# Kernel optimization log

Measured on AMD Instinct MI355X. Metric: run time of the kernel, lower is better.

The kernel has to match this reference:

```python
import jax, jax.numpy as jnp
import numpy as np

DIM = 2048
K_DIM = 2048
HQ = 16          # query heads
HKV = 4          # kv heads
HD = DIM // HQ   # head dim = 128
KV_DIM = HD * HKV
MAX_LEN = 4096
THETA = 10000.0
ROPE_FACTOR = 8.0
CAUSAL = True
SCALE = HD ** -0.5


def rope_cos_sin(n):
    # mirrors generate_sin_cos_pos_emb (rope_factor > 1 branch)
    idx = jnp.arange(0, HD, 2, dtype=jnp.float32) / HD
    seq_len_eff = max(n, MAX_LEN)  # static python ints
    base_adjustment = (ROPE_FACTOR * seq_len_eff / MAX_LEN - (ROPE_FACTOR - 1.0)) ** (HD / (HD - 2))
    inv_freq = 1.0 / (THETA * base_adjustment) ** idx
    pos = jnp.arange(n, dtype=jnp.float32)
    if not CAUSAL:
        pos = pos - (n - 1) // 2
    freqs = pos[:, None] * inv_freq[None, :]          # [n, HD/2]
    emb = jnp.concatenate([freqs, freqs], axis=-1)    # [n, HD]
    return jnp.cos(emb), jnp.sin(emb)


def rotate_half(x):
    x1, x2 = jnp.split(x, 2, axis=-1)
    return jnp.concatenate([-x2, x1], axis=-1)


def setup_inputs() -> dict:
    key = jax.random.key(0)
    ks = jax.random.split(key, 11)
    B, N = 2, 2048
    s = 0.02
    return {
        "query": jax.random.normal(ks[0], (B, N, DIM), jnp.float32),
        "key": jax.random.normal(ks[1], (B, N, K_DIM), jnp.float32),
        "value": jax.random.normal(ks[2], (B, N, K_DIM), jnp.float32),
        "Wq": jax.random.normal(ks[3], (DIM, DIM), jnp.float32) * s,
        "bq": jnp.zeros((DIM,), jnp.float32),
        "Wk": jax.random.normal(ks[4], (KV_DIM, K_DIM), jnp.float32) * s,
        "bk": jnp.zeros((KV_DIM,), jnp.float32),
        "Wv": jax.random.normal(ks[5], (KV_DIM, K_DIM), jnp.float32) * s,
        "bv": jnp.zeros((KV_DIM,), jnp.float32),
        "Wo": jax.random.normal(ks[6], (DIM, DIM), jnp.float32) * s,
        "bo": jnp.zeros((DIM,), jnp.float32),
    }


def reference(query, key, value, Wq, bq, Wk, bk, Wv, bv, Wo, bo):
    b, n, _ = query.shape
    q = query @ Wq.T + bq                       # [b, n, DIM]
    k = key @ Wk.T + bk                         # [b, n, KV_DIM]
    v = value @ Wv.T + bv                       # [b, n, KV_DIM]
    q = q.reshape(b, n, HQ, HD).transpose(0, 2, 1, 3)    # [b, HQ, n, d]
    k = k.reshape(b, n, HKV, HD).transpose(0, 2, 1, 3)   # [b, HKV, n, d]
    v = v.reshape(b, n, HKV, HD).transpose(0, 2, 1, 3)
    cos, sin = rope_cos_sin(n)                  # [n, HD] each, broadcast over b,h
    q = q * cos + rotate_half(q) * sin
    k = k * cos + rotate_half(k) * sin
    g = HQ // HKV
    qg = q.reshape(b, HKV, g, n, HD)            # group query heads per kv head
    scores = jnp.einsum('bhgnd,bhsd->bhgns', qg * SCALE, k)  # [b, HKV, g, n, s]
    if CAUSAL:
        causal = jnp.tril(jnp.ones((n, n), dtype=bool))
        scores = jnp.where(causal[None, None, None], scores, jnp.finfo(scores.dtype).min)
    attn = jax.nn.softmax(scores, axis=-1)
    out = jnp.einsum('bhgns,bhsd->bhgnd', attn, v)           # [b, HKV, g, n, d]
    out = out.reshape(b, HQ, n, HD).transpose(0, 2, 1, 3).reshape(b, n, DIM)
    return out @ Wo.T + bo
```

## Files before the change

kernel.cpp:

```cpp
#include <hip/hip_runtime.h>
#include <cstdint>


typedef __bf16 bf16_t;
typedef __attribute__((ext_vector_type(8))) __bf16 bf16x8;
typedef __attribute__((ext_vector_type(4))) float f32x4;

#define B_    2
#define N_    2048
#define DIM_  2048
#define HQ_   16
#define HKV_  4
#define HD_   128
#define KVD_  512
#define SCALE_ 0.08838834764831845f

static __device__ __forceinline__ void ld_g2l(void* lds, const void* g) {
  __builtin_amdgcn_global_load_lds((__attribute__((address_space(1))) void*)g,
                                   (__attribute__((address_space(3))) void*)lds,
                                   16, 0, 0);
}

static __device__ __forceinline__ f32x4 vmax4(f32x4 a, f32x4 b) {
  f32x4 r;
  r[0] = fmaxf(a[0], b[0]); r[1] = fmaxf(a[1], b[1]);
  r[2] = fmaxf(a[2], b[2]); r[3] = fmaxf(a[3], b[3]);
  return r;
}

__global__ void k_prep(float* __restrict__ cosT, float* __restrict__ sinT,
                       const float* __restrict__ s0, bf16_t* __restrict__ d0, int n0,
                       const float* __restrict__ s1, bf16_t* __restrict__ d1, int n1,
                       const float* __restrict__ s2, bf16_t* __restrict__ d2, int n2,
                       const float* __restrict__ s3, bf16_t* __restrict__ d3, int n3)
{
  if (blockIdx.x < 512) {
    int idx = blockIdx.x * 256 + threadIdx.x;
    int i = idx & 63;
    int n = idx >> 6;
    float inv = expf(-(float)i * (9.210340371976184f / 64.0f));
    float ang = (float)n * inv;
    cosT[idx] = cosf(ang);
    sinT[idx] = sinf(ang);
    return;
  }
  int i = ((blockIdx.x - 512) * 256 + threadIdx.x) * 4;
  const float* s; bf16_t* d; int off;
  if (i < n0)                     { s = s0; d = d0; off = i; }
  else if (i < n0 + n1)           { s = s1; d = d1; off = i - n0; }
  else if (i < n0 + n1 + n2)      { s = s2; d = d2; off = i - n0 - n1; }
  else if (i < n0 + n1 + n2 + n3) { s = s3; d = d3; off = i - n0 - n1 - n2; }
  else return;
  f32x4 v = *(const f32x4*)(s + off);
  union { bf16_t h[4]; uint2 u; } pk;
  pk.h[0] = (bf16_t)v[0]; pk.h[1] = (bf16_t)v[1];
  pk.h[2] = (bf16_t)v[2]; pk.h[3] = (bf16_t)v[3];
  *(uint2*)(d + off) = pk.u;
}

__global__ __launch_bounds__(256, 2) void k_gemm_qkv(
    const float* __restrict__ q, const bf16_t* __restrict__ Wqb,
    const float* __restrict__ bq, bf16_t* __restrict__ Qp,
    const float* __restrict__ k, const bf16_t* __restrict__ Wkb,
    const float* __restrict__ bk, bf16_t* __restrict__ Kp,
    const float* __restrict__ v, const bf16_t* __restrict__ Wvb,
    const float* __restrict__ bv, bf16_t* __restrict__ Vp)
{
  __shared__ bf16_t As[128 * 64];
  __shared__ bf16_t Bs[2][128 * 64];
  const int z = blockIdx.z;
  if (z != 0 && blockIdx.y >= 2) return;
  const float* A; const bf16_t* W; const float* bias; bf16_t* C; int Nn;
  if (z == 0)      { A = q; W = Wqb; bias = bq; C = Qp; Nn = 2048; }
  else if (z == 1) { A = k; W = Wkb; bias = bk; C = Kp; Nn = 512; }
  else             { A = v; W = Wvb; bias = bv; C = Vp; Nn = 512; }

  const int tid  = threadIdx.x;
  const int lane = tid & 63;
  const int wave = tid >> 6;
  const int l15  = lane & 15;
  const int lg   = lane >> 4;
  const int bm = blockIdx.x;
  const int bn0 = blockIdx.y * 2, bn1 = bn0 + 1;
  const int wr = (wave >> 1) * 64, wc = (wave & 1) * 64;
  const int K = 2048;

  f32x4 acc0[4][4] = {};
  f32x4 acc1[4][4] = {};

  uint8_t* AsB = (uint8_t*)As;
  uint8_t* Bs0 = (uint8_t*)Bs[0];
  uint8_t* Bs1 = (uint8_t*)Bs[1];
  const uint8_t* Wb0 = (const uint8_t*)W + (size_t)(bn0 * 128) * K * 2;
  const uint8_t* Wb1 = (const uint8_t*)W + (size_t)(bn1 * 128) * K * 2;

  f32x4 arLo[4], arHi[4];

  auto loadA = [&](int k0) {
#pragma unroll
    for (int i = 0; i < 4; ++i) {
      int c = i * 256 + tid;
      int row = c >> 3;
      int k8  = (c & 7) * 8;
      const float* ap = A + (size_t)(bm * 128 + row) * K + k0 + k8;
      arLo[i] = *(const f32x4*)ap;
      arHi[i] = *(const f32x4*)(ap + 4);
    }
  };
  auto writeA = [&]() {
#pragma unroll
    for (int i = 0; i < 4; ++i) {
      int c = i * 256 + tid;
      int row = c >> 3;
      int k8  = (c & 7) * 8;
      bf16x8 va;
      f32x4 lo = arLo[i], hi = arHi[i];
      va[0] = (bf16_t)lo[0]; va[1] = (bf16_t)lo[1];
      va[2] = (bf16_t)lo[2]; va[3] = (bf16_t)lo[3];
      va[4] = (bf16_t)hi[0]; va[5] = (bf16_t)hi[1];
      va[6] = (bf16_t)hi[2]; va[7] = (bf16_t)hi[3];
      int sw = (k8 * 2) ^ ((row & 7) << 4);
      *(bf16x8*)(AsB + row * 128 + sw) = va;
    }
  };

  loadA(0);

  for (int k0 = 0; k0 < K; k0 += 64) {
#pragma unroll
    for (int r = 0; r < 4; ++r) {
      int o = r * 4096 + wave * 1024 + lane * 16;
      int row = o >> 7;
      int colB = (o & 127) ^ ((row & 7) << 4);
      size_t goff = (size_t)row * (K * 2) + (size_t)k0 * 2 + colB;
      ld_g2l(Bs0 + r * 4096 + wave * 1024, Wb0 + goff);
      ld_g2l(Bs1 + r * 4096 + wave * 1024, Wb1 + goff);
    }
    writeA();
    const bool more = (k0 + 64 < K);
    __syncthreads();
    if (more) loadA(k0 + 64);
    __builtin_amdgcn_s_setprio(1);
#pragma unroll
    for (int kk = 0; kk < 2; ++kk) {
      const int koff = kk * 64 + (lg << 4);
      bf16x8 fa[4], fb[4];
#pragma unroll
      for (int fi = 0; fi < 4; ++fi) {
        int row = wr + fi * 16 + l15;
        fa[fi] = *(const bf16x8*)(AsB + row * 128 + (koff ^ ((row & 7) << 4)));
      }
#pragma unroll
      for (int fj = 0; fj < 4; ++fj) {
        int row = wc + fj * 16 + l15;
        fb[fj] = *(const bf16x8*)(Bs0 + row * 128 + (koff ^ ((row & 7) << 4)));
      }
#pragma unroll
      for (int fi = 0; fi < 4; ++fi)
#pragma unroll
        for (int fj = 0; fj < 4; ++fj)
          acc0[fi][fj] = __builtin_amdgcn_mfma_f32_16x16x32_bf16(
              fa[fi], fb[fj], acc0[fi][fj], 0, 0, 0);
#pragma unroll
      for (int fj = 0; fj < 4; ++fj) {
        int row = wc + fj * 16 + l15;
        fb[fj] = *(const bf16x8*)(Bs1 + row * 128 + (koff ^ ((row & 7) << 4)));
      }
#pragma unroll
      for (int fi = 0; fi < 4; ++fi)
#pragma unroll
        for (int fj = 0; fj < 4; ++fj)
          acc1[fi][fj] = __builtin_amdgcn_mfma_f32_16x16x32_bf16(
              fa[fi], fb[fj], acc1[fi][fj], 0, 0, 0);
    }
    __builtin_amdgcn_s_setprio(0);
    __syncthreads();
  }

  const int r0 = lg * 4;
#pragma unroll
  for (int fi = 0; fi < 4; ++fi) {
#pragma unroll
    for (int rr = 0; rr < 4; ++rr) {
      int grow = bm * 128 + wr + fi * 16 + r0 + rr;
      size_t rowoff = (size_t)grow * Nn;
#pragma unroll
      for (int fj = 0; fj < 4; ++fj) {
        int gc0 = bn0 * 128 + wc + fj * 16 + l15;
        int gc1 = bn1 * 128 + wc + fj * 16 + l15;
        C[rowoff + gc0] = (bf16_t)(acc0[fi][fj][rr] + bias[gc0]);
        C[rowoff + gc1] = (bf16_t)(acc1[fi][fj][rr] + bias[gc1]);
      }
    }
  }
}

__global__ __launch_bounds__(256, 4) void k_gemm_o(
    const bf16_t* __restrict__ Ain, const bf16_t* __restrict__ Wob,
    const float* __restrict__ bo, float* __restrict__ out)
{
  __shared__ bf16_t As[128 * 64];
  __shared__ bf16_t Bs[128 * 64];
  const int tid  = threadIdx.x;
  const int lane = tid & 63;
  const int wave = tid >> 6;
  const int l15  = lane & 15;
  const int lg   = lane >> 4;
  const int bm = blockIdx.x, bn = blockIdx.y;
  const int wr = (wave >> 1) * 64, wc = (wave & 1) * 64;
  const int K = 2048, N = 2048;

  f32x4 acc[4][4] = {};
  uint8_t* AsB = (uint8_t*)As;
  uint8_t* BsB = (uint8_t*)Bs;
  const uint8_t* Wbase = (const uint8_t*)Wob + (size_t)(bn * 128) * K * 2;
  const uint8_t* Abase = (const uint8_t*)Ain + (size_t)(bm * 128) * K * 2;

  for (int k0 = 0; k0 < K; k0 += 64) {
    for (int r = 0; r < 4; ++r) {
      int o = r * 4096 + wave * 1024 + lane * 16;
      int row = o >> 7;
      int colB = (o & 127) ^ ((row & 7) << 4);
      size_t goff = (size_t)row * (K * 2) + (size_t)k0 * 2 + colB;
      ld_g2l(BsB + r * 4096 + wave * 1024, Wbase + goff);
      ld_g2l(AsB + r * 4096 + wave * 1024, Abase + goff);
    }
    __syncthreads();
    for (int kk = 0; kk < 2; ++kk) {
      const int koff = kk * 64 + (lg << 4);
      bf16x8 fa[4], fb[4];
      for (int fi = 0; fi < 4; ++fi) {
        int row = wr + fi * 16 + l15;
        fa[fi] = *(const bf16x8*)(AsB + row * 128 + (koff ^ ((row & 7) << 4)));
      }
      for (int fj = 0; fj < 4; ++fj) {
        int row = wc + fj * 16 + l15;
        fb[fj] = *(const bf16x8*)(BsB + row * 128 + (koff ^ ((row & 7) << 4)));
      }
      for (int fi = 0; fi < 4; ++fi)
        for (int fj = 0; fj < 4; ++fj)
          acc[fi][fj] = __builtin_amdgcn_mfma_f32_16x16x32_bf16(
              fa[fi], fb[fj], acc[fi][fj], 0, 0, 0);
    }
    __syncthreads();
  }

  const int r0 = lg * 4;
  for (int fi = 0; fi < 4; ++fi) {
    for (int rr = 0; rr < 4; ++rr) {
      int grow = bm * 128 + wr + fi * 16 + r0 + rr;
      size_t rowoff = (size_t)grow * N;
      for (int fj = 0; fj < 4; ++fj) {
        int gcol = bn * 128 + wc + fj * 16 + l15;
        out[rowoff + gcol] = acc[fi][fj][rr] + bo[gcol];
      }
    }
  }
}

__global__ void k_ropek_transv(bf16_t* __restrict__ Kp,
                               const float* __restrict__ cosT,
                               const float* __restrict__ sinT,
                               const bf16_t* __restrict__ Vp,
                               bf16_t* __restrict__ Vt)
{
  __shared__ bf16_t tile[64][72];
  const int tid = threadIdx.x;
  if (blockIdx.x < 512) {
    int idx = blockIdx.x * 256 + tid;
    int j = idx & 7;
    int h = (idx >> 3) & 3;
    int row = idx >> 5;
    int n = row & (N_ - 1);
    int d0 = j * 8;
    const float* cp = cosT + (n << 6) + d0;
    const float* sp = sinT + (n << 6) + d0;
    f32x4 c0 = *(const f32x4*)cp,  c1 = *(const f32x4*)(cp + 4);
    f32x4 s0 = *(const f32x4*)sp,  s1 = *(const f32x4*)(sp + 4);
    bf16_t* xb = Kp + (size_t)row * 512 + (h << 7) + d0;
    bf16x8 x1 = *(const bf16x8*)xb;
    bf16x8 x2 = *(const bf16x8*)(xb + 64);
    bf16x8 o1, o2;
#pragma unroll
    for (int e = 0; e < 8; ++e) {
      float c = e < 4 ? c0[e] : c1[e - 4];
      float s = e < 4 ? s0[e] : s1[e - 4];
      float a = (float)x1[e], bvl = (float)x2[e];
      o1[e] = (bf16_t)(a * c - bvl * s);
      o2[e] = (bf16_t)(bvl * c + a * s);
    }
    *(bf16x8*)xb = o1;
    *(bf16x8*)(xb + 64) = o2;
    return;
  }
  const int bid = blockIdx.x - 512;
  const int r0 = (bid & 63) * 64;
  const int d0 = (bid >> 6) * 64;
  for (int r = 0; r < 2; ++r) {
    int n = r * 32 + (tid >> 3);
    int dc = (tid & 7) * 8;
    *(uint4*)&tile[n][dc] = *(const uint4*)(Vp + (size_t)(r0 + n) * KVD_ + d0 + dc);
  }
  __syncthreads();
  const int b = r0 >> 11;
  const int nseq = r0 & (N_ - 1);
  for (int r = 0; r < 2; ++r) {
    int dd = r * 32 + (tid >> 3);
    int nc = (tid & 7) * 8;
    int dglob = d0 + dd;
    int hkv = dglob >> 7, dloc = dglob & 127;
    union { bf16_t h[8]; uint4 v; } pk;
    for (int j = 0; j < 8; ++j) pk.h[j] = tile[nc + j][dd];
    size_t drow = (size_t)(b * HKV_ + hkv) * 128 + dloc;
    *(uint4*)(Vt + drow * N_ + nseq + nc) = pk.v;
  }
}

__global__ __launch_bounds__(256, 2) void k_attn(
    const bf16_t* __restrict__ Qp, const bf16_t* __restrict__ Kp,
    const bf16_t* __restrict__ Vt, bf16_t* __restrict__ AO,
    const float* __restrict__ cosT, const float* __restrict__ sinT)
{
  __shared__ bf16_t Ks[2][64 * 128];
  __shared__ bf16_t Vs[2][128 * 64];
  __shared__ bf16_t Ps[4][16 * 72];
  const int tid = threadIdx.x, lane = tid & 63, wave = tid >> 6;
  const int l15 = lane & 15, lg = lane >> 4;
  const int bx = (blockIdx.y < 16) ? (15 - (int)blockIdx.x) : (int)blockIdx.x;
  const int qtile = bx * 4 + wave;
  const int bh = blockIdx.y;
  const int b = bh >> 4, hq = bh & 15, hkv = hq >> 2;

  bf16x8 qf[2][4];
#pragma unroll
  for (int rf = 0; rf < 2; ++rf) {
    int n = qtile * 32 + rf * 16 + l15;
    size_t qrow = (size_t)b * N_ + n;
    const uint8_t* qb = (const uint8_t*)Qp + (qrow * DIM_ + (size_t)hq * HD_) * 2 + lg * 16;
#pragma unroll
    for (int ks = 0; ks < 4; ++ks)
      qf[rf][ks] = *(const bf16x8*)(qb + ks * 64);
    const float* cb = cosT + n * 64 + lg * 8;
    const float* sb = sinT + n * 64 + lg * 8;
    f32x4 c0a = *(const f32x4*)cb,        c0b = *(const f32x4*)(cb + 4);
    f32x4 c1a = *(const f32x4*)(cb + 32), c1b = *(const f32x4*)(cb + 36);
    f32x4 s0a = *(const f32x4*)sb,        s0b = *(const f32x4*)(sb + 4);
    f32x4 s1a = *(const f32x4*)(sb + 32), s1b = *(const f32x4*)(sb + 36);
#pragma unroll
    for (int e = 0; e < 8; ++e) {
      float c0 = e < 4 ? c0a[e] : c0b[e - 4], s0 = e < 4 ? s0a[e] : s0b[e - 4];
      float c1 = e < 4 ? c1a[e] : c1b[e - 4], s1 = e < 4 ? s1a[e] : s1b[e - 4];
      float a0 = (float)qf[rf][0][e], b0 = (float)qf[rf][2][e];
      float a1 = (float)qf[rf][1][e], b1 = (float)qf[rf][3][e];
      qf[rf][0][e] = (bf16_t)((a0 * c0 - b0 * s0) * SCALE_);
      qf[rf][2][e] = (bf16_t)((b0 * c0 + a0 * s0) * SCALE_);
      qf[rf][1][e] = (bf16_t)((a1 * c1 - b1 * s1) * SCALE_);
      qf[rf][3][e] = (bf16_t)((b1 * c1 + a1 * s1) * SCALE_);
    }
  }

  float m[2] = {-1e30f, -1e30f};
  float ln[2] = {0.f, 0.f};
  f32x4 o[2][8] = {};

  const uint8_t* KpB = (const uint8_t*)Kp + ((size_t)b * N_ * KVD_ + (size_t)hkv * HD_) * 2;
  const uint8_t* VtB = (const uint8_t*)Vt + (size_t)(b * HKV_ + hkv) * HD_ * (size_t)N_ * 2;
  uint8_t* PwB = (uint8_t*)Ps[wave];

  const int Tw   = qtile / 2 + 1;
  const int Tmax = 2 * bx + 2;

  auto stage = [&](int buf, int t) {
    uint8_t* KsB = (uint8_t*)Ks[buf];
    uint8_t* VsB = (uint8_t*)Vs[buf];
#pragma unroll
    for (int r = 0; r < 4; ++r) {
      int o16 = r * 4096 + wave * 1024 + lane * 16;
      int row = o16 >> 8;
      int colB = (o16 & 255) ^ ((row & 7) << 4);
      ld_g2l(KsB + r * 4096 + wave * 1024,
             KpB + (size_t)(t * 64 + row) * (KVD_ * 2) + colB);
    }
#pragma unroll
    for (int r = 0; r < 4; ++r) {
      int o16 = r * 4096 + wave * 1024 + lane * 16;
      int dd = o16 >> 7;
      int colB = (o16 & 127) ^ ((dd & 7) << 4);
      ld_g2l(VsB + r * 4096 + wave * 1024,
             VtB + (size_t)dd * (N_ * 2) + t * 128 + colB);
    }
  };

  stage(0, 0);
  __syncthreads();
  int cur = 0;

  for (int t = 0; t < Tmax; ++t) {
    if (t + 1 < Tmax) stage(cur ^ 1, t + 1);

    if (t < Tw) {
      const uint8_t* KsB = (const uint8_t*)Ks[cur];
      const uint8_t* VsB = (const uint8_t*)Vs[cur];

      f32x4 s4[2][4] = {};
      __builtin_amdgcn_s_setprio(1);
#pragma unroll
      for (int ks = 0; ks < 4; ++ks) {
        int koff = ks * 64 + lg * 16;
#pragma unroll
        for (int kb = 0; kb < 4; ++kb) {
          int row = kb * 16 + l15;
          bf16x8 kf = *(const bf16x8*)(KsB + row * 256 + (koff ^ ((row & 7) << 4)));
          s4[0][kb] = __builtin_amdgcn_mfma_f32_16x16x32_bf16(kf, qf[0][ks], s4[0][kb], 0, 0, 0);
          s4[1][kb] = __builtin_amdgcn_mfma_f32_16x16x32_bf16(kf, qf[1][ks], s4[1][kb], 0, 0, 0);
        }
      }
      __builtin_amdgcn_s_setprio(0);

      if (t == Tw - 1) {
#pragma unroll
        for (int rf = 0; rf < 2; ++rf) {
          int q = qtile * 32 + rf * 16 + l15;
#pragma unroll
          for (int kb = 0; kb < 4; ++kb) {
            int key = t * 64 + kb * 16 + lg * 4;
#pragma unroll
            for (int rr = 0; rr < 4; ++rr)
              if (key + rr > q) s4[rf][kb][rr] = -1e30f;
          }
        }
      }

      bf16x8 pf[2][2];
#pragma unroll
      for (int rf = 0; rf < 2; ++rf) {
        f32x4 mx = vmax4(vmax4(s4[rf][0], s4[rf][1]), vmax4(s4[rf][2], s4[rf][3]));
        float rm = fmaxf(fmaxf(mx[0], mx[1]), fmaxf(mx[2], mx[3]));
        rm = fmaxf(rm, __shfl_xor(rm, 16));
        rm = fmaxf(rm, __shfl_xor(rm, 32));

        const bool defer = __all(rm <= m[rf] + 8.0f);
        float mn = defer ? m[rf] : fmaxf(m[rf], rm);
        float sc = defer ? 1.0f : __expf(m[rf] - mn);

        f32x4 p[4];
        f32x4 psum = {0.f, 0.f, 0.f, 0.f};
#pragma unroll
        for (int kb = 0; kb < 4; ++kb) {
#pragma unroll
          for (int rr = 0; rr < 4; ++rr)
            p[kb][rr] = __expf(s4[rf][kb][rr] - mn);
          psum += p[kb];
        }
        float rs = (psum[0] + psum[1]) + (psum[2] + psum[3]);
        rs += __shfl_xor(rs, 16);
        rs += __shfl_xor(rs, 32);
        ln[rf] = ln[rf] * sc + rs;
        m[rf] = mn;

        if (!defer) {
#pragma unroll
          for (int db = 0; db < 8; ++db) o[rf][db] *= sc;
        }

#pragma unroll
        for (int kb = 0; kb < 4; ++kb) {
          union { bf16_t h[4]; uint2 u; } pk;
          pk.h[0] = (bf16_t)p[kb][0]; pk.h[1] = (bf16_t)p[kb][1];
          pk.h[2] = (bf16_t)p[kb][2]; pk.h[3] = (bf16_t)p[kb][3];
          *(uint2*)(PwB + l15 * 144 + kb * 32 + lg * 8) = pk.u;
        }
        pf[rf][0] = *(const bf16x8*)(PwB + l15 * 144 + lg * 16);
        pf[rf][1] = *(const bf16x8*)(PwB + l15 * 144 + 64 + lg * 16);
      }

      __builtin_amdgcn_s_setprio(1);
#pragma unroll
      for (int ks2 = 0; ks2 < 2; ++ks2) {
        int koff = ks2 * 64 + lg * 16;
#pragma unroll
        for (int db = 0; db < 8; ++db) {
          int dd = db * 16 + l15;
          bf16x8 vf = *(const bf16x8*)(VsB + dd * 128 + (koff ^ ((dd & 7) << 4)));
          o[0][db] = __builtin_amdgcn_mfma_f32_16x16x32_bf16(vf, pf[0][ks2], o[0][db], 0, 0, 0);
          o[1][db] = __builtin_amdgcn_mfma_f32_16x16x32_bf16(vf, pf[1][ks2], o[1][db], 0, 0, 0);
        }
      }
      __builtin_amdgcn_s_setprio(0);
    }

    __syncthreads();
    cur ^= 1;
  }

#pragma unroll
  for (int rf = 0; rf < 2; ++rf) {
    float iv = 1.f / ln[rf];
    size_t qrow = (size_t)b * N_ + qtile * 32 + rf * 16 + l15;
    uint8_t* ob = (uint8_t*)(AO + qrow * DIM_ + (size_t)hq * HD_);
#pragma unroll
    for (int db = 0; db < 8; ++db) {
      union { bf16_t h[4]; uint2 u; } pk;
      pk.h[0] = (bf16_t)(o[rf][db][0] * iv);
      pk.h[1] = (bf16_t)(o[rf][db][1] * iv);
      pk.h[2] = (bf16_t)(o[rf][db][2] * iv);
      pk.h[3] = (bf16_t)(o[rf][db][3] * iv);
      *(uint2*)(ob + (db * 16 + lg * 4) * 2) = pk.u;
    }
  }
}

extern "C" void kernel_launch(void* const* d_in, const int* in_sizes, int n_in,
                              void* d_out, int out_size, void* d_ws, size_t ws_size,
                              hipStream_t stream)
{
  if (ws_size < (46u << 20)) return;

  const float* query = (const float*)d_in[0];
  const float* key   = (const float*)d_in[1];
  const float* value = (const float*)d_in[2];
  const float* Wq = (const float*)d_in[3];
  const float* bq = (const float*)d_in[4];
  const float* Wk = (const float*)d_in[5];
  const float* bk = (const float*)d_in[6];
  const float* Wv = (const float*)d_in[7];
  const float* bv = (const float*)d_in[8];
  const float* Wo = (const float*)d_in[9];
  const float* bo = (const float*)d_in[10];
  float* out = (float*)d_out;

  uint8_t* ws = (uint8_t*)d_ws;
  float*  cosT = (float*)(ws);
  float*  sinT = (float*)(ws + (512u << 10));
  bf16_t* Qp   = (bf16_t*)(ws + (1u  << 20));
  bf16_t* Kp   = (bf16_t*)(ws + (17u << 20));
  bf16_t* Vp   = (bf16_t*)(ws + (21u << 20));
  bf16_t* Vt   = (bf16_t*)(ws + (25u << 20));
  bf16_t* Wqb  = (bf16_t*)(ws + (29u << 20));
  bf16_t* Wkb  = (bf16_t*)(ws + (37u << 20));
  bf16_t* Wvb  = (bf16_t*)(ws + (39u << 20));
  bf16_t* WobL = (bf16_t*)(ws + (17u << 20));
  bf16_t* WobE = (bf16_t*)(ws + (41u << 20));

  const bool bigws = ws_size >= (50ull << 20);

  if (bigws) {
    k_prep<<<512 + 10240, 256, 0, stream>>>(cosT, sinT,
                                            Wq, Wqb, 4194304,
                                            Wk, Wkb, 1048576,
                                            Wv, Wvb, 1048576,
                                            Wo, WobE, 4194304);
  } else {
    k_prep<<<512 + 6144, 256, 0, stream>>>(cosT, sinT,
                                           Wq, Wqb, 4194304,
                                           Wk, Wkb, 1048576,
                                           Wv, Wvb, 1048576,
                                           nullptr, nullptr, 0);
  }

  k_gemm_qkv<<<dim3(32, 8, 3), 256, 0, stream>>>(
      query, Wqb, bq, Qp, key, Wkb, bk, Kp, value, Wvb, bv, Vp);

  k_ropek_transv<<<1024, 256, 0, stream>>>(Kp, cosT, sinT, Vp, Vt);

  k_attn<<<dim3(16, 32), 256, 0, stream>>>(Qp, Kp, Vt, Qp, cosT, sinT);

  if (!bigws) {
    k_prep<<<4096, 256, 0, stream>>>(nullptr, nullptr,
                                     Wo, WobL, 4194304,
                                     nullptr, nullptr, 0,
                                     nullptr, nullptr, 0,
                                     nullptr, nullptr, 0);
  }

  k_gemm_o<<<dim3(32, 16), 256, 0, stream>>>(
      Qp, bigws ? WobE : WobL, bo, out);
}
```

Baseline: 199.3 us.

## Fuse K RoPE and V transpose into QKV GEMM epilogue

Removes the separate RoPE-on-K and V-transpose kernel by doing both in the QKV projection's epilogue through an LDS staging tile. K blocks apply rotary embedding using the partner half read from shared memory, and V blocks write the transposed layout directly. This saves a kernel launch and a round trip of K and V through global memory, but it adds barriers and strided LDS reads to the GEMM epilogue. The small-workspace Wo buffer is moved so it no longer overlaps Kp.

```diff
diff --git a/kernel.cpp b/kernel.cpp
--- a/kernel.cpp
+++ b/kernel.cpp
@@ -64,16 +64,16 @@
     const float* __restrict__ k, const bf16_t* __restrict__ Wkb,
     const float* __restrict__ bk, bf16_t* __restrict__ Kp,
     const float* __restrict__ v, const bf16_t* __restrict__ Wvb,
-    const float* __restrict__ bv, bf16_t* __restrict__ Vp)
+    const float* __restrict__ bv, bf16_t* __restrict__ Vt,
+    const float* __restrict__ cosT, const float* __restrict__ sinT)
 {
-  __shared__ bf16_t As[128 * 64];
-  __shared__ bf16_t Bs[2][128 * 64];
+  __shared__ bf16_t smem[24576];
   const int z = blockIdx.z;
   if (z != 0 && blockIdx.y >= 2) return;
-  const float* A; const bf16_t* W; const float* bias; bf16_t* C; int Nn;
-  if (z == 0)      { A = q; W = Wqb; bias = bq; C = Qp; Nn = 2048; }
-  else if (z == 1) { A = k; W = Wkb; bias = bk; C = Kp; Nn = 512; }
-  else             { A = v; W = Wvb; bias = bv; C = Vp; Nn = 512; }
+  const float* A; const bf16_t* W; const float* bias;
+  if (z == 0)      { A = q; W = Wqb; bias = bq; }
+  else if (z == 1) { A = k; W = Wkb; bias = bk; }
+  else             { A = v; W = Wvb; bias = bv; }
 
   const int tid  = threadIdx.x;
   const int lane = tid & 63;
@@ -88,9 +88,9 @@
   f32x4 acc0[4][4] = {};
   f32x4 acc1[4][4] = {};
 
-  uint8_t* AsB = (uint8_t*)As;
-  uint8_t* Bs0 = (uint8_t*)Bs[0];
-  uint8_t* Bs1 = (uint8_t*)Bs[1];
+  uint8_t* AsB = (uint8_t*)smem;
+  uint8_t* Bs0 = AsB + 16384;
+  uint8_t* Bs1 = AsB + 32768;
   const uint8_t* Wb0 = (const uint8_t*)W + (size_t)(bn0 * 128) * K * 2;
   const uint8_t* Wb1 = (const uint8_t*)W + (size_t)(bn1 * 128) * K * 2;
 
@@ -178,20 +178,79 @@
   }
 
   const int r0 = lg * 4;
-#pragma unroll
-  for (int fi = 0; fi < 4; ++fi) {
-#pragma unroll
-    for (int rr = 0; rr < 4; ++rr) {
-      int grow = bm * 128 + wr + fi * 16 + r0 + rr;
-      size_t rowoff = (size_t)grow * Nn;
-#pragma unroll
-      for (int fj = 0; fj < 4; ++fj) {
-        int gc0 = bn0 * 128 + wc + fj * 16 + l15;
-        int gc1 = bn1 * 128 + wc + fj * 16 + l15;
-        C[rowoff + gc0] = (bf16_t)(acc0[fi][fj][rr] + bias[gc0]);
-        C[rowoff + gc1] = (bf16_t)(acc1[fi][fj][rr] + bias[gc1]);
-      }
-    }
+
+  if (z == 0) {
+#pragma unroll
+    for (int fi = 0; fi < 4; ++fi)
+#pragma unroll
+      for (int rr = 0; rr < 4; ++rr) {
+        int grow = bm * 128 + wr + fi * 16 + r0 + rr;
+        size_t rowoff = (size_t)grow * 2048;
+#pragma unroll
+        for (int fj = 0; fj < 4; ++fj) {
+          int gc0 = bn0 * 128 + wc + fj * 16 + l15;
+          int gc1 = bn1 * 128 + wc + fj * 16 + l15;
+          Qp[rowoff + gc0] = (bf16_t)(acc0[fi][fj][rr] + bias[gc0]);
+          Qp[rowoff + gc1] = (bf16_t)(acc1[fi][fj][rr] + bias[gc1]);
+        }
+      }
+    return;
+  }
+
+  bf16_t* T = smem;
+  const int nbase = (bm * 128) & (N_ - 1);
+  const int vb = (bm * 128) >> 11;
+
+  for (int t = 0; t < 2; ++t) {
+    const int bn = t == 0 ? bn0 : bn1;
+    f32x4 (&acc)[4][4] = t == 0 ? acc0 : acc1;
+
+#pragma unroll
+    for (int fi = 0; fi < 4; ++fi)
+#pragma unroll
+      for (int rr = 0; rr < 4; ++rr) {
+        int row = wr + fi * 16 + r0 + rr;
+#pragma unroll
+        for (int fj = 0; fj < 4; ++fj) {
+          int d = wc + fj * 16 + l15;
+          T[row * 132 + d] = (bf16_t)(acc[fi][fj][rr] + bias[bn * 128 + d]);
+        }
+      }
+    __syncthreads();
+
+    if (z == 1) {
+#pragma unroll
+      for (int fi = 0; fi < 4; ++fi)
+#pragma unroll
+        for (int rr = 0; rr < 4; ++rr) {
+          int row = wr + fi * 16 + r0 + rr;
+          int grow = bm * 128 + row;
+          int n = grow & (N_ - 1);
+#pragma unroll
+          for (int fj = 0; fj < 4; ++fj) {
+            int d = wc + fj * 16 + l15;
+            float own = acc[fi][fj][rr] + bias[bn * 128 + d];
+            float p = (float)T[row * 132 + (d ^ 64)];
+            int di = d & 63;
+            float c = cosT[n * 64 + di];
+            float s = sinT[n * 64 + di];
+            float outv = (d < 64) ? (own * c - p * s) : (own * c + p * s);
+            Kp[(size_t)grow * KVD_ + bn * 128 + d] = (bf16_t)outv;
+          }
+        }
+    } else {
+#pragma unroll
+      for (int j = 0; j < 8; ++j) {
+        int e = j * 256 + tid;
+        int d = e >> 4;
+        int nc = (e & 15) * 8;
+        union { bf16_t h[8]; uint4 u; } pk;
+#pragma unroll
+        for (int i = 0; i < 8; ++i) pk.h[i] = T[(nc + i) * 132 + d];
+        *(uint4*)(Vt + ((size_t)((vb * HKV_ + bn) * 128 + d)) * N_ + nbase + nc) = pk.u;
+      }
+    }
+    __syncthreads();
   }
 }
 
@@ -258,64 +317,6 @@
   }
 }
 
-__global__ void k_ropek_transv(bf16_t* __restrict__ Kp,
-                               const float* __restrict__ cosT,
-                               const float* __restrict__ sinT,
-                               const bf16_t* __restrict__ Vp,
-                               bf16_t* __restrict__ Vt)
-{
-  __shared__ bf16_t tile[64][72];
-  const int tid = threadIdx.x;
-  if (blockIdx.x < 512) {
-    int idx = blockIdx.x * 256 + tid;
-    int j = idx & 7;
-    int h = (idx >> 3) & 3;
-    int row = idx >> 5;
-    int n = row & (N_ - 1);
-    int d0 = j * 8;
-    const float* cp = cosT + (n << 6) + d0;
-    const float* sp = sinT + (n << 6) + d0;
-    f32x4 c0 = *(const f32x4*)cp,  c1 = *(const f32x4*)(cp + 4);
-    f32x4 s0 = *(const f32x4*)sp,  s1 = *(const f32x4*)(sp + 4);
-    bf16_t* xb = Kp + (size_t)row * 512 + (h << 7) + d0;
-    bf16x8 x1 = *(const bf16x8*)xb;
-    bf16x8 x2 = *(const bf16x8*)(xb + 64);
-    bf16x8 o1, o2;
-#pragma unroll
-    for (int e = 0; e < 8; ++e) {
-      float c = e < 4 ? c0[e] : c1[e - 4];
-      float s = e < 4 ? s0[e] : s1[e - 4];
-      float a = (float)x1[e], bvl = (float)x2[e];
-      o1[e] = (bf16_t)(a * c - bvl * s);
-      o2[e] = (bf16_t)(bvl * c + a * s);
-    }
-    *(bf16x8*)xb = o1;
-    *(bf16x8*)(xb + 64) = o2;
-    return;
-  }
-  const int bid = blockIdx.x - 512;
-  const int r0 = (bid & 63) * 64;
-  const int d0 = (bid >> 6) * 64;
-  for (int r = 0; r < 2; ++r) {
-    int n = r * 32 + (tid >> 3);
-    int dc = (tid & 7) * 8;
-    *(uint4*)&tile[n][dc] = *(const uint4*)(Vp + (size_t)(r0 + n) * KVD_ + d0 + dc);
-  }
-  __syncthreads();
-  const int b = r0 >> 11;
-  const int nseq = r0 & (N_ - 1);
-  for (int r = 0; r < 2; ++r) {
-    int dd = r * 32 + (tid >> 3);
-    int nc = (tid & 7) * 8;
-    int dglob = d0 + dd;
-    int hkv = dglob >> 7, dloc = dglob & 127;
-    union { bf16_t h[8]; uint4 v; } pk;
-    for (int j = 0; j < 8; ++j) pk.h[j] = tile[nc + j][dd];
-    size_t drow = (size_t)(b * HKV_ + hkv) * 128 + dloc;
-    *(uint4*)(Vt + drow * N_ + nseq + nc) = pk.v;
-  }
-}
-
 __global__ __launch_bounds__(256, 2) void k_attn(
     const bf16_t* __restrict__ Qp, const bf16_t* __restrict__ Kp,
     const bf16_t* __restrict__ Vt, bf16_t* __restrict__ AO,
@@ -534,12 +535,11 @@
   float*  sinT = (float*)(ws + (512u << 10));
   bf16_t* Qp   = (bf16_t*)(ws + (1u  << 20));
   bf16_t* Kp   = (bf16_t*)(ws + (17u << 20));
-  bf16_t* Vp   = (bf16_t*)(ws + (21u << 20));
   bf16_t* Vt   = (bf16_t*)(ws + (25u << 20));
   bf16_t* Wqb  = (bf16_t*)(ws + (29u << 20));
   bf16_t* Wkb  = (bf16_t*)(ws + (37u << 20));
   bf16_t* Wvb  = (bf16_t*)(ws + (39u << 20));
-  bf16_t* WobL = (bf16_t*)(ws + (17u << 20));
+  bf16_t* WobL = (bf16_t*)(ws + (17u << 20) + (4u << 20));
   bf16_t* WobE = (bf16_t*)(ws + (41u << 20));
 
   const bool bigws = ws_size >= (50ull << 20);
@@ -559,9 +559,7 @@
   }
 
   k_gemm_qkv<<<dim3(32, 8, 3), 256, 0, stream>>>(
-      query, Wqb, bq, Qp, key, Wkb, bk, Kp, value, Wvb, bv, Vp);
-
-  k_ropek_transv<<<1024, 256, 0, stream>>>(Kp, cosT, sinT, Vp, Vt);
+      query, Wqb, bq, Qp, key, Wkb, bk, Kp, value, Wvb, bv, Vt, cosT, sinT);
 
   k_attn<<<dim3(16, 32), 256, 0, stream>>>(Qp, Kp, Vt, Qp, cosT, sinT);
 
```

Result: slower. 229.0 us (+14.9%).
